# Kernel optimization log

Hardware: AMD Instinct MI355X
Metric: run time of the kernel (lower is better)

Reference implementation:

```python
import jax, jax.numpy as jnp
import numpy as np

N = 4096; IN = 78; OUT = 11
HN = 256; HB = 128; HM = 64; HV = 256; HU = 128
NOTES_PER_BEAT = 8; BEATS_PER_MEASURE = 4
NB = N // NOTES_PER_BEAT; NM = NB // BEATS_PER_MEASURE
UIN = 2*HN + 2*HB + 2*HM + 2*HV + OUT + 2 + 1 + 2   # output-LSTM input = 1424
BT_IN = 2*HB + 1 + 1 + 2 + 3 + (OUT - 1)            # tempo-LSTM input = 273
QPM_PRIMO_IDX = 5; TEMPO_IDX = 28


def _u(key, shape, k):
    return jax.random.uniform(key, shape, minval=-k, maxval=k, dtype=jnp.float32)


def _lstm_p(key, din, h, bidir):
    k = 1.0 / np.sqrt(h); n = 2 if bidir else 1
    k1, k2, k3 = jax.random.split(key, 3)
    Wi = _u(k1, (n, 4*h, din), k); Wh = _u(k2, (n, 4*h, h), k); b = _u(k3, (n, 4*h), k)
    if not bidir:
        Wi, Wh, b = Wi[0], Wh[0], b[0]
    return Wi, Wh, b


def _lin_p(key, din, dout):
    k = 1.0 / np.sqrt(din)
    k1, k2 = jax.random.split(key)
    return _u(k1, (dout, din), k), _u(k2, (dout,), k)


def setup_inputs():
    ks = jax.random.split(jax.random.key(0), 20)
    inp = {}
    inp['x'] = jax.random.normal(ks[0], (1, N, IN), dtype=jnp.float32)
    inp['y'] = jax.random.normal(ks[1], (1, 1, OUT), dtype=jnp.float32)
    inp['beat_ids'] = (jnp.arange(N) // NOTES_PER_BEAT).astype(jnp.int32)
    inp['measure_ids'] = (jnp.arange(N) // (NOTES_PER_BEAT * BEATS_PER_MEASURE)).astype(jnp.int32)
    inp['note_Wi'], inp['note_Wh'], inp['note_b'] = _lstm_p(ks[2], IN, HN, True)
    inp['voice_Wi'], inp['voice_Wh'], inp['voice_b'] = _lstm_p(ks[3], IN, HV, True)
    inp['beat_Wi'], inp['beat_Wh'], inp['beat_b'] = _lstm_p(ks[4], 2*HN, HB, True)
    inp['meas_Wi'], inp['meas_Wh'], inp['meas_b'] = _lstm_p(ks[5], 2*HB, HM, True)
    inp['Wba'], inp['bba'] = _lin_p(ks[6], 2*HN, 2*HN)
    inp['Wma'], inp['bma'] = _lin_p(ks[7], 2*HB, 2*HB)
    inp['Wta'], inp['bta'] = _lin_p(ks[8], OUT-1, OUT-1)
    inp['out_Wi'], inp['out_Wh'], inp['out_b'] = _lstm_p(ks[9], UIN, HU, False)
    inp['Wfc'], inp['bfc'] = _lin_p(ks[10], HU + UIN, OUT-1)
    inp['bt_Wi'], inp['bt_Wh'], inp['bt_b'] = _lstm_p(ks[11], BT_IN, HB, False)
    inp['Wt1'], inp['bt1'] = _lin_p(ks[12], HB, HB)
    inp['Wt2'], inp['bt2'] = _lin_p(ks[13], HB, 1)
    return inp


def _cell(h, c, xt, Wi, Wh, b):
    g = Wi @ xt + Wh @ h + b
    i, f, gg, o = jnp.split(g, 4)
    c2 = jax.nn.sigmoid(f) * c + jax.nn.sigmoid(i) * jnp.tanh(gg)
    return jax.nn.sigmoid(o) * jnp.tanh(c2), c2


def _lstm(xs, Wi, Wh, b, reverse=False):
    H = Wh.shape[-1]
    def step(carry, xt):
        h, c = _cell(carry[0], carry[1], xt, Wi, Wh, b)
        return (h, c), h
    init = (jnp.zeros(H, xs.dtype), jnp.zeros(H, xs.dtype))
    _, hs = jax.lax.scan(step, init, xs, reverse=reverse)
    return hs


def _bilstm(xs, Wi, Wh, b):
    return jnp.concatenate([_lstm(xs, Wi[0], Wh[0], b[0]),
                            _lstm(xs, Wi[1], Wh[1], b[1], reverse=True)], axis=-1)


def _seg_attn(h, seg, nseg, W, b):
    # sum_with_attention: softmax over group members, per feature dim (torch softmax dim=0)
    logits = h @ W.T + b
    m = jax.ops.segment_max(logits, seg, num_segments=nseg)
    e = jnp.exp(logits - m[seg])
    s = jax.ops.segment_sum(e, seg, num_segments=nseg)
    return jax.ops.segment_sum(h * (e / s[seg]), seg, num_segments=nseg)


def _forward(x, y, beat_ids, measure_ids, note_Wi, note_Wh, note_b, voice_Wi, voice_Wh, voice_b,
             beat_Wi, beat_Wh, beat_b, meas_Wi, meas_Wh, meas_b, Wba, bba, Wma, bma, Wta, bta,
             out_Wi, out_Wh, out_b, Wfc, bfc, bt_Wi, bt_Wh, bt_b, Wt1, bt1, Wt2, bt2):
    xs = x[0]                                   # [N, IN]
    note_h = _bilstm(xs, note_Wi, note_Wh, note_b)          # [N, 2*HN]
    voice_h = _bilstm(xs, voice_Wi, voice_Wh, voice_b)      # single voice -> whole seq
    beat_nodes = _seg_attn(note_h, beat_ids, NB, Wba, bba)  # [NB, 2*HN]
    beat_h = _bilstm(beat_nodes, beat_Wi, beat_Wh, beat_b)  # [NB, 2*HB]
    meas_of_beat = jax.ops.segment_min(measure_ids, beat_ids, num_segments=NB)
    meas_nodes = _seg_attn(beat_h, meas_of_beat, NM, Wma, bma)
    meas_h = _bilstm(meas_nodes, meas_Wi, meas_Wh, meas_b)  # [NM, 2*HM]

    qpm_primo = x[:, 0, QPM_PRIMO_IDX]          # (1,)
    tempo_primo = x[0, 0, -2:]                  # (2,)
    btv = xs[:, TEMPO_IDX:TEMPO_IDX+3]          # [N, 3]
    beat_pn = beat_h[beat_ids]                  # [N, 2*HB]
    meas_pn = meas_h[measure_ids]               # [N, 2*HM]
    is_b = jnp.concatenate([jnp.array([True]), beat_ids[1:] > beat_ids[:-1]])
    y_tail = y[0, 0, 1:]

    def step(carry, inp):
        buf, count, pt, th, tc, oh, oc, po, pv = carry
        nh_i, bh_i, mh_i, vh_i, btv_i, isb = inp
        # --- beat boundary: tempo attention + tempo LSTM step ---
        mask = jnp.arange(NOTES_PER_BEAT) < count
        logits = jnp.where(mask[:, None], buf @ Wta.T + bta, -1e9)
        att = jax.nn.softmax(logits, axis=0)
        result_node = jnp.where(count > 0, jnp.sum(buf * att, axis=0), y_tail)
        cat = jnp.concatenate([bh_i, pt, qpm_primo, tempo_primo, btv_i, result_node])
        nth, ntc = _cell(th, tc, cat, bt_Wi, bt_Wh, bt_b)
        tmp = Wt2 @ jax.nn.relu(Wt1 @ nth + bt1) + bt2     # (1,)
        th = jnp.where(isb, nth, th); tc = jnp.where(isb, ntc, tc)
        pt = jnp.where(isb, tmp, pt)
        buf = jnp.where(isb, jnp.zeros_like(buf), buf)
        count = jnp.where(isb, 0, count)
        comb = jnp.concatenate([nh_i, bh_i, mh_i, vh_i, po, pv, qpm_primo, tempo_primo])  # (UIN,)
        noh, noc = _cell(oh, oc, comb, out_Wi, out_Wh, out_b)
        out_fc = Wfc @ jnp.concatenate([noh, comb]) + bfc   # (OUT-1,)
        out = jnp.concatenate([pt, out_fc])                 # (OUT,)
        buf = buf.at[count].set(out_fc)
        return (buf, count + 1, pt, th, tc, noh, noc, out, out_fc[:2]), out

    carry0 = (jnp.zeros((NOTES_PER_BEAT, OUT-1)), jnp.array(0, jnp.int32), y[:, 0, 0],
              jnp.zeros(HB), jnp.zeros(HB), jnp.zeros(HU), jnp.zeros(HU), y[0, 0, :], jnp.zeros(2))
    _, outs = jax.lax.scan(step, carry0, (note_h, beat_pn, meas_pn, voice_h, btv, is_b))
    return outs[None], note_h[None]


def reference(x, y, beat_ids, measure_ids, note_Wi, note_Wh, note_b, voice_Wi, voice_Wh, voice_b,
              beat_Wi, beat_Wh, beat_b, meas_Wi, meas_Wh, meas_b, Wba, bba, Wma, bma, Wta, bta,
              out_Wi, out_Wh, out_b, Wfc, bfc, bt_Wi, bt_Wh, bt_b, Wt1, bt1, Wt2, bt2):
    return _forward(x, y, beat_ids, measure_ids, note_Wi, note_Wh, note_b, voice_Wi, voice_Wh, voice_b,
                    beat_Wi, beat_Wh, beat_b, meas_Wi, meas_Wh, meas_b, Wba, bba, Wma, bma, Wta, bta,
                    out_Wi, out_Wh, out_b, Wfc, bfc, bt_Wi, bt_Wh, bt_b, Wt1, bt1, Wt2, bt2)
```

## Files before the change

### kernel.cpp

```cpp
#include <hip/hip_runtime.h>
#include <hip/hip_bf16.h>

typedef unsigned int u32;
typedef _Float16 h16;
typedef __attribute__((ext_vector_type(2))) _Float16 h16x2;

union U4 { uint4 u; h16x2 p[4]; };

static __device__ __forceinline__ float sigm(float x){ return 1.0f / (1.0f + __expf(-x)); }
static __device__ __forceinline__ float ftanh(float x){ return 1.0f - 2.0f/(1.0f + __expf(2.0f*x)); }
static __device__ __forceinline__ h16x2 f2h2(float a, float b){
  h16x2 r; r[0] = (h16)a; r[1] = (h16)b; return r;
}
static __device__ __forceinline__ void pinv(h16x2 &x){
  u32 t = __builtin_bit_cast(u32, x);
  asm volatile("" : "+v"(t));
  x = __builtin_bit_cast(h16x2, t);
}

#if defined(__has_builtin)
#if __has_builtin(__builtin_amdgcn_fdot2)
#define FDOT2_NATIVE 1
#endif
#endif
static __device__ __forceinline__ float fdot2(h16x2 a, h16x2 b, float c){
#ifdef FDOT2_NATIVE
  return __builtin_amdgcn_fdot2(a, b, c, false);
#else
  return c + (float)a[0]*(float)b[0] + (float)a[1]*(float)b[1];
#endif
}

#define NT 4096
#define OUTS_OFF 45056

__global__ __launch_bounds__(256) void k0_prep(
    const float* __restrict__ noteWh, const float* __restrict__ voiceWh,
    const float* __restrict__ outWi,  const float* __restrict__ Wfc,
    h16* __restrict__ WhF, h16* __restrict__ outWiF, h16* __restrict__ WfcKF)
{
  const int NWH = 4*1024*256;
  const int NOW = 512*1416;
  const int NFC = 10*1416;
  for (int i = blockIdx.x*256 + threadIdx.x; i < NWH + NOW + NFC; i += gridDim.x*256) {
    if (i < NWH) {
      int dir = i >> 18;
      int rem = i & 262143;
      const float* src = (dir < 2) ? noteWh : voiceWh;
      WhF[i] = (h16)src[((dir & 1) << 18) + rem];
    } else if (i < NWH + NOW) {
      int j = i - NWH;
      int r = j / 1416, c = j - r*1416;
      float v = 0.f;
      if (c < 1408) v = outWi[(size_t)r*1424 + c];
      else if (c < 1411) v = outWi[(size_t)r*1424 + 1421 + (c-1408)];
      outWiF[j] = (h16)v;
    } else {
      int j = i - NWH - NOW;
      int r = j / 1416, c = j - r*1416;
      float v = 0.f;
      if (c < 1408) v = Wfc[(size_t)r*1552 + 128 + c];
      else if (c < 1411) v = Wfc[(size_t)r*1552 + 1549 + (c-1408)];
      WfcKF[j] = (h16)v;
    }
  }
}

__global__ __launch_bounds__(256) void k1_xgates(
    const float* __restrict__ x,
    const float* __restrict__ noteWi, const float* __restrict__ noteB,
    const float* __restrict__ voiceWi, const float* __restrict__ voiceB,
    h16* __restrict__ preNV)
{
  const int dir = blockIdx.y;
  const int t0  = blockIdx.x * 16;
  const int tid = threadIdx.x;
  __shared__ float xs[16][80];
  for (int i = tid; i < 16*78; i += 256) {
    int tt = i / 78, j = i - tt*78;
    xs[tt][j] = x[(size_t)(t0+tt)*78 + j];
  }
  __syncthreads();
  const float* Wi = (dir < 2) ? noteWi : voiceWi;
  const float* B  = (dir < 2) ? noteB  : voiceB;
  const int dw = dir & 1;
  for (int gc = 0; gc < 4; ++gc) {
    int g = gc*256 + tid;
    const float* row = Wi + ((size_t)dw*1024 + g)*78;
    float bias = B[dw*1024 + g];
    float acc[16];
#pragma unroll
    for (int tt=0; tt<16; ++tt) acc[tt] = bias;
#pragma unroll 6
    for (int j=0; j<78; ++j) {
      float w = row[j];
#pragma unroll
      for (int tt=0; tt<16; ++tt)
        acc[tt] += w*xs[tt][j];
    }
#pragma unroll
    for (int tt=0; tt<16; ++tt)
      preNV[((size_t)dir*NT + (t0+tt))*1024 + (tid*4 + gc)] = (h16)acc[tt];
  }
}

__global__ __launch_bounds__(512, 2) void k2_nvrec(
    const h16* __restrict__ WhF,
    const h16* __restrict__ preNV,
    float* __restrict__ note_h,
    float* __restrict__ voice_h,
    float* __restrict__ out_noteh)
{
  const int dir = blockIdx.x;
  const int L = threadIdx.x;
  const int lane = L & 63;
  const int wid  = L >> 6;
  const int hi   = lane >> 5;
  const int e    = wid*32 + (lane & 31);
  const int c0   = hi*128;
  const h16* Wb = WhF + (size_t)dir*1024*256;

  h16x2 w[4][48];
#pragma unroll
  for (int g=0; g<4; ++g) {
    const h16* row = Wb + (size_t)(g*256 + e)*256 + c0;
#pragma unroll
    for (int cb=0; cb<12; ++cb) {
      U4 a; a.u = *(const uint4*)(row + cb*8);
#pragma unroll
      for (int i=0;i<4;++i) w[g][cb*4+i] = a.p[i];
    }
  }
#pragma unroll
  for (int g=0; g<4; ++g)
#pragma unroll
    for (int c=0;c<48;++c) pinv(w[g][c]);

  __shared__ __align__(16) h16 Wl[4*4*2*256*8];
  __shared__ __align__(16) h16 hb[2][256];
#pragma unroll
  for (int cb=0; cb<4; ++cb)
#pragma unroll
    for (int g=0; g<4; ++g) {
      const h16* src = Wb + (size_t)(g*256 + e)*256 + c0 + 96 + cb*8;
      *(uint4*)&Wl[(size_t)((((cb*4+g)*2 + hi)*256 + e))*8] = *(const uint4*)src;
    }
  if (hi == 0) hb[0][e] = (h16)0.f;
  float cc = 0.f;
  __syncthreads();

  const bool fwd = ((dir & 1) == 0);
  const bool isNote = (dir < 2);
  float* hout = isNote ? note_h : voice_h;
  const int half = (dir & 1) * 256;
  const h16* pre = preNV + (size_t)dir*NT*1024;
  int cur = 0;
  const int step = fwd ? 1 : -1;
  int t = fwd ? 0 : NT-1;

  union PU { uint2 u; h16 h[4]; };
  PU pv_n; pv_n.u = *(const uint2*)(pre + (size_t)t*1024 + e*4);

  for (int it = 0; it < NT; ++it, t += step) {
    PU pv = pv_n;
    if (it+1 < NT) pv_n.u = *(const uint2*)(pre + (size_t)(t+step)*1024 + e*4);

    float ac[4][2] = {{0.f,0.f},{0.f,0.f},{0.f,0.f},{0.f,0.f}};
#pragma unroll
    for (int cb=0; cb<12; ++cb) {
      U4 hh; hh.u = *(const uint4*)&hb[cur][c0 + cb*8];
#pragma unroll
      for (int i=0;i<4;++i) {
        ac[0][i&1] = fdot2(w[0][cb*4+i], hh.p[i], ac[0][i&1]);
        ac[1][i&1] = fdot2(w[1][cb*4+i], hh.p[i], ac[1][i&1]);
        ac[2][i&1] = fdot2(w[2][cb*4+i], hh.p[i], ac[2][i&1]);
        ac[3][i&1] = fdot2(w[3][cb*4+i], hh.p[i], ac[3][i&1]);
      }
    }
#pragma unroll
    for (int cb=0; cb<4; ++cb) {
      U4 hh; hh.u = *(const uint4*)&hb[cur][c0 + 96 + cb*8];
#pragma unroll
      for (int g=0; g<4; ++g) {
        U4 wv; wv.u = *(const uint4*)&Wl[(size_t)((((cb*4+g)*2 + hi)*256 + e))*8];
#pragma unroll
        for (int i=0;i<4;++i) ac[g][i&1] = fdot2(wv.p[i], hh.p[i], ac[g][i&1]);
      }
    }
    float g4[4];
#pragma unroll
    for (int g=0; g<4; ++g) {
      float s = ac[g][0] + ac[g][1];
      s += __shfl_xor(s, 32, 64);
      g4[g] = s;
    }
    float gi = (float)pv.h[0] + g4[0];
    float gf = (float)pv.h[1] + g4[1];
    float gg = (float)pv.h[2] + g4[2];
    float go = (float)pv.h[3] + g4[3];
    cc = sigm(gf)*cc + sigm(gi)*ftanh(gg);
    float h = sigm(go)*ftanh(cc);
    if (hi == 0) {
      hb[cur^1][e] = (h16)h;
      hout[(size_t)t*512 + half + e] = h;
      if (isNote) out_noteh[(size_t)t*512 + half + e] = h;
    }
    cur ^= 1;
    __syncthreads();
  }
}

__global__ __launch_bounds__(256) void k3_battn(
    const float* __restrict__ note_h,
    const float* __restrict__ Wba, const float* __restrict__ bba,
    float* __restrict__ beat_nodes)
{
  const int b = blockIdx.x;
  const int tid = threadIdx.x;
  __shared__ float nh[8][512];
  for (int i = tid; i < 8*512; i += 256)
    nh[i>>9][i&511] = note_h[(size_t)b*8*512 + i];
  __syncthreads();
  for (int dc = 0; dc < 2; ++dc) {
    int d = dc*256 + tid;
    const float* wr = Wba + (size_t)d*512;
    float bb = bba[d];
    float l[8];
#pragma unroll
    for (int n=0;n<8;++n) l[n]=bb;
#pragma unroll 4
    for (int j=0; j<512; ++j) {
      float w = wr[j];
#pragma unroll
      for (int n=0;n<8;++n) l[n] += w*nh[n][j];
    }
    float m = l[0];
#pragma unroll
    for (int n=1;n<8;++n) m = fmaxf(m, l[n]);
    float s = 0.f, o = 0.f;
#pragma unroll
    for (int n=0;n<8;++n) { float e = __expf(l[n]-m); s += e; o += e*nh[n][d]; }
    beat_nodes[(size_t)b*512 + d] = o / s;
  }
}

__global__ __launch_bounds__(256) void k4_bgates(
    const float* __restrict__ beat_nodes,
    const float* __restrict__ beatWi, const float* __restrict__ beatB,
    float* __restrict__ preB)
{
  const int dir = blockIdx.y, b0 = blockIdx.x*8, tid = threadIdx.x;
  __shared__ float nd[8][512];
  for (int i = tid; i < 8*512; i += 256)
    nd[i>>9][i&511] = beat_nodes[(size_t)b0*512 + i];
  __syncthreads();
  for (int gc = 0; gc < 2; ++gc) {
    int g = gc*256 + tid;
    const float* wr = beatWi + ((size_t)dir*512 + g)*512;
    float bias = beatB[dir*512 + g];
    float acc[8];
#pragma unroll
    for (int n=0;n<8;++n) acc[n]=bias;
#pragma unroll 4
    for (int j=0; j<512; ++j) {
      float w = wr[j];
#pragma unroll
      for (int n=0;n<8;++n) acc[n] += w*nd[n][j];
    }
#pragma unroll
    for (int n=0;n<8;++n)
      preB[((size_t)dir*512 + (b0+n))*512 + g] = acc[n];
  }
}

__global__ __launch_bounds__(512) void k5_brec(
    const float* __restrict__ beatWh,
    const float* __restrict__ preB,
    float* __restrict__ beat_h)
{
  const int dir = blockIdx.x, L = threadIdx.x;
  h16x2 w[64];
  {
    const float2* p = (const float2*)(beatWh + ((size_t)dir*512 + L)*128);
#pragma unroll
    for (int c=0;c<64;++c){
      float2 v = p[c];
      w[c] = f2h2(v.x, v.y);
    }
  }
#pragma unroll
  for (int c=0;c<64;++c) pinv(w[c]);
  __shared__ __align__(16) h16 hb[128];
  __shared__ float gl[512];
  if (L < 128) hb[L] = (h16)0.f;
  float cc = 0.f;
  __syncthreads();
  const bool fwd = (dir == 0);
  for (int it = 0; it < 512; ++it) {
    const int t = fwd ? it : 511 - it;
    float pr = preB[((size_t)dir*512 + t)*512 + L];
    float ac[4] = {0.f,0.f,0.f,0.f};
#pragma unroll
    for (int c=0;c<16;++c){
      U4 hh; hh.u = *(const uint4*)&hb[c*8];
#pragma unroll
      for (int i=0;i<4;++i) ac[i] = fdot2(w[c*4+i], hh.p[i], ac[i]);
    }
    gl[L] = pr + ((ac[0]+ac[1]) + (ac[2]+ac[3]));
    __syncthreads();
    if (L < 128) {
      float gi = gl[L], gf = gl[L+128], gg = gl[L+256], go = gl[L+384];
      cc = sigm(gf)*cc + sigm(gi)*ftanh(gg);
      float h = sigm(go)*ftanh(cc);
      hb[L] = (h16)h;
      beat_h[(size_t)t*256 + dir*128 + L] = h;
    }
    __syncthreads();
  }
}

__global__ __launch_bounds__(256) void k6_mattn(
    const float* __restrict__ beat_h,
    const float* __restrict__ Wma, const float* __restrict__ bma,
    float* __restrict__ meas_nodes)
{
  const int m = blockIdx.x, tid = threadIdx.x;
  __shared__ float bh[4][256];
  for (int i = tid; i < 4*256; i += 256)
    bh[i>>8][i&255] = beat_h[(size_t)m*4*256 + i];
  __syncthreads();
  int d = tid;
  const float* wr = Wma + (size_t)d*256;
  float bb = bma[d];
  float l[4];
#pragma unroll
  for (int n=0;n<4;++n) l[n]=bb;
#pragma unroll 4
  for (int j=0; j<256; ++j) {
    float w = wr[j];
#pragma unroll
    for (int n=0;n<4;++n) l[n] += w*bh[n][j];
  }
  float mm = fmaxf(fmaxf(l[0],l[1]), fmaxf(l[2],l[3]));
  float s = 0.f, o = 0.f;
#pragma unroll
  for (int n=0;n<4;++n) { float e = __expf(l[n]-mm); s += e; o += e*bh[n][d]; }
  meas_nodes[(size_t)m*256 + d] = o / s;
}

__global__ __launch_bounds__(256) void k7_mgates(
    const float* __restrict__ meas_nodes,
    const float* __restrict__ measWi, const float* __restrict__ measB,
    float* __restrict__ preM)
{
  const int dir = blockIdx.y, m0 = blockIdx.x*8, tid = threadIdx.x;
  __shared__ float nd[8][256];
  for (int i = tid; i < 8*256; i += 256)
    nd[i>>8][i&255] = meas_nodes[(size_t)m0*256 + i];
  __syncthreads();
  int g = tid;
  const float* wr = measWi + ((size_t)dir*256 + g)*256;
  float bias = measB[dir*256 + g];
  float acc[8];
#pragma unroll
  for (int n=0;n<8;++n) acc[n]=bias;
#pragma unroll 4
  for (int j=0; j<256; ++j) {
    float w = wr[j];
#pragma unroll
    for (int n=0;n<8;++n) acc[n] += w*nd[n][j];
  }
#pragma unroll
  for (int n=0;n<8;++n)
    preM[((size_t)dir*128 + (m0+n))*256 + g] = acc[n];
}

__global__ __launch_bounds__(256, 2) void k8_mrec(
    const float* __restrict__ measWh,
    const float* __restrict__ preM,
    float* __restrict__ meas_h)
{
  const int dir = blockIdx.x, L = threadIdx.x;
  h16x2 w[32];
  {
    const float2* p = (const float2*)(measWh + ((size_t)dir*256 + L)*64);
#pragma unroll
    for (int c=0;c<32;++c){
      float2 v = p[c];
      w[c] = f2h2(v.x, v.y);
    }
  }
#pragma unroll
  for (int c=0;c<32;++c) pinv(w[c]);
  __shared__ __align__(16) h16 hb[64];
  __shared__ float gl[256];
  if (L < 64) hb[L] = (h16)0.f;
  float cc = 0.f;
  __syncthreads();
  const bool fwd = (dir == 0);
  for (int it = 0; it < 128; ++it) {
    const int t = fwd ? it : 127 - it;
    float pr = preM[((size_t)dir*128 + t)*256 + L];
    float ac[4] = {0.f,0.f,0.f,0.f};
#pragma unroll
    for (int c=0;c<8;++c){
      U4 hh; hh.u = *(const uint4*)&hb[c*8];
#pragma unroll
      for (int i=0;i<4;++i) ac[i] = fdot2(w[c*4+i], hh.p[i], ac[i]);
    }
    gl[L] = pr + ((ac[0]+ac[1]) + (ac[2]+ac[3]));
    __syncthreads();
    if (L < 64) {
      float gi = gl[L], gf = gl[L+64], gg = gl[L+128], go = gl[L+192];
      cc = sigm(gf)*cc + sigm(gi)*ftanh(gg);
      float h = sigm(go)*ftanh(cc);
      hb[L] = (h16)h;
      meas_h[(size_t)t*128 + dir*64 + L] = h;
    }
    __syncthreads();
  }
}

__global__ __launch_bounds__(256) void k9_scanpre(
    const float* __restrict__ note_h, const float* __restrict__ voice_h,
    const float* __restrict__ beat_h, const float* __restrict__ meas_h,
    const float* __restrict__ xf,
    const h16* __restrict__ outWiF, const h16* __restrict__ WfcKF,
    const float* __restrict__ outB, const float* __restrict__ bfc,
    float* __restrict__ pre_out, float* __restrict__ pre_fc)
{
  const int t0 = blockIdx.x*8, tid = threadIdx.x;
  __shared__ __align__(16) h16 kn[8][1416];
  const float qpm = xf[5], tp0 = xf[76], tp1 = xf[77];
  for (int i = tid; i < 8*1416; i += 256) {
    int tt = i/1416, c = i - tt*1416;
    int t = t0 + tt;
    float v;
    if (c < 512) v = note_h[(size_t)t*512 + c];
    else if (c < 768) v = beat_h[(size_t)(t>>3)*256 + (c-512)];
    else if (c < 896) v = meas_h[(size_t)(t>>5)*128 + (c-768)];
    else if (c < 1408) v = voice_h[(size_t)t*512 + (c-896)];
    else if (c == 1408) v = qpm;
    else if (c == 1409) v = tp0;
    else if (c == 1410) v = tp1;
    else v = 0.f;
    kn[tt][c] = (h16)v;
  }
  __syncthreads();
  for (int rr = 0; rr < 3; ++rr) {
    int r = (rr < 2) ? (tid + rr*256) : (512 + tid);
    if (rr == 2 && tid >= 10) break;
    const h16* wrow = (r < 512) ? (outWiF + (size_t)r*1416) : (WfcKF + (size_t)(r-512)*1416);
    float bias = (r < 512) ? outB[r] : bfc[r-512];
    float acc[8];
#pragma unroll
    for (int tt=0;tt<8;++tt) acc[tt] = bias;
    for (int cu = 0; cu < 177; ++cu) {
      U4 wv; wv.u = *(const uint4*)(wrow + cu*8);
#pragma unroll
      for (int tt=0; tt<8; ++tt) {
        U4 kv; kv.u = *(const uint4*)&kn[tt][cu*8];
#pragma unroll
        for (int i=0;i<4;++i) acc[tt] = fdot2(wv.p[i], kv.p[i], acc[tt]);
      }
    }
#pragma unroll
    for (int tt=0; tt<8; ++tt) {
      if (r < 512) pre_out[(size_t)(t0+tt)*512 + r] = acc[tt];
      else pre_fc[(size_t)(t0+tt)*16 + (r-512)] = acc[tt];
    }
  }
}

__global__ __launch_bounds__(256) void k9b_btpre(
    const float* __restrict__ beat_h, const float* __restrict__ xf,
    const float* __restrict__ btWi, const float* __restrict__ btB,
    float* __restrict__ pre_bt)
{
  const int b0 = blockIdx.x*8, tid = threadIdx.x;
  __shared__ float bh[8][256];
  __shared__ float btv[8][3];
  for (int i = tid; i < 8*256; i += 256)
    bh[i>>8][i&255] = beat_h[(size_t)b0*256 + i];
  if (tid < 24) {
    int n = tid/3, j = tid - n*3;
    btv[n][j] = xf[(size_t)(b0+n)*8*78 + 28 + j];
  }
  __syncthreads();
  const float qpm = xf[5], tp0 = xf[76], tp1 = xf[77];
  for (int gc = 0; gc < 2; ++gc) {
    int g = gc*256 + tid;
    const float* row = btWi + (size_t)g*273;
    float bias = btB[g];
    float acc[8];
#pragma unroll
    for (int n=0;n<8;++n) acc[n]=bias;
#pragma unroll 4
    for (int j = 0; j < 256; ++j) {
      float w = row[j];
#pragma unroll
      for (int n=0;n<8;++n) acc[n] += w*bh[n][j];
    }
    float w257 = row[257], w258 = row[258], w259 = row[259];
    float w260 = row[260], w261 = row[261], w262 = row[262];
#pragma unroll
    for (int n=0;n<8;++n) {
      acc[n] += w257*qpm + w258*tp0 + w259*tp1
              + w260*btv[n][0] + w261*btv[n][1] + w262*btv[n][2];
      pre_bt[(size_t)(b0+n)*512 + g] = acc[n];
    }
  }
}

__global__ __launch_bounds__(512) void k10_scan(
    const float* __restrict__ pre_out, const float* __restrict__ pre_fc,
    const float* __restrict__ pre_bt,
    const float* __restrict__ outWh, const float* __restrict__ btWh,
    const float* __restrict__ outWi, const float* __restrict__ btWi,
    const float* __restrict__ Wfc,
    const float* __restrict__ Wta, const float* __restrict__ bta,
    const float* __restrict__ Wt1, const float* __restrict__ bt1,
    const float* __restrict__ Wt2, const float* __restrict__ bt2,
    const float* __restrict__ yf,
    float* __restrict__ out)
{
  const int L = threadIdx.x;
  h16x2 owh[64], btw[64];
  {
    const float2* p = (const float2*)(outWh + (size_t)L*128);
    const float2* q = (const float2*)(btWh + (size_t)L*128);
#pragma unroll
    for (int c=0;c<64;++c){
      float2 a = p[c]; owh[c] = f2h2(a.x, a.y);
      float2 b = q[c]; btw[c] = f2h2(b.x, b.y);
    }
  }
#pragma unroll
  for (int c=0;c<64;++c){ pinv(owh[c]); pinv(btw[c]); }
  float oseq[13];
#pragma unroll
  for (int j=0;j<13;++j) oseq[j] = outWi[(size_t)L*1424 + 1408 + j];
  float btpt = btWi[(size_t)L*273 + 256];
  float btrn[10];
#pragma unroll
  for (int d=0;d<10;++d) btrn[d] = btWi[(size_t)L*273 + 263 + d];

  __shared__ __align__(16) h16 oh16[128];
  __shared__ __align__(16) h16 th16[128];
  __shared__ __align__(16) h16 Wt1f[128*136];
  __shared__ __align__(16) h16 WfcD[10*128];
  __shared__ float gl[512], gb[512];
  __shared__ float pofc[16];
  __shared__ float ptvS;
  __shared__ float buf[8][10];
  __shared__ float rn[10], att[8][10], r1v[128], ytail[10];
  __shared__ float WfcSeq[10][13];
  __shared__ float WtaS[100], btaS[10], Wt2S[128], bt1S[128], bt2S;

  for (int i=L; i<128*128; i+=512) Wt1f[(i>>7)*136 + (i&127)] = (h16)Wt1[i];
  for (int i=L; i<10*128; i+=512)  WfcD[i] = (h16)Wfc[(size_t)(i>>7)*1552 + (i&127)];
  if (L < 100) WtaS[L] = Wta[L];
  if (L < 10)  btaS[L] = bta[L];
  if (L < 128) { Wt2S[L] = Wt2[L]; bt1S[L] = bt1[L]; }
  if (L == 0)  bt2S = bt2[0];
  if (L < 128) { oh16[L] = (h16)0.f; th16[L] = (h16)0.f; }
  if (L < 11) pofc[L] = yf[L];
  if (L >= 11 && L < 16) pofc[L] = 0.f;
  if (L == 0) ptvS = yf[0];
  if (L < 10) ytail[L] = yf[1+L];
  if (L < 80) buf[L/10][L%10] = 0.f;
  if (L < 130) WfcSeq[L/13][L%13] = Wfc[(size_t)(L/13)*1552 + 1536 + (L%13)];
  float oc = 0.f, tc = 0.f;
  const int dD = L >> 2, qD = L & 3;
  float prv  = pre_out[L];
  float prbt = pre_bt[L];
  float prfc = (L < 40 && qD == 0) ? pre_fc[dD] : 0.f;
  __syncthreads();

  for (int t = 0; t < NT; ++t) {
    const bool isb = (t & 7) == 0;
    if (isb) {
      if (t == 0) {
        if (L < 10) rn[L] = ytail[L];
      } else {
        if (L < 80) {
          int n = L/10, d = L - n*10;
          float s = btaS[d];
#pragma unroll
          for (int j=0;j<10;++j) s += buf[n][j]*WtaS[d*10 + j];
          att[n][d] = s;
        }
        __syncthreads();
        if (L < 10) {
          float m = att[0][L];
#pragma unroll
          for (int n=1;n<8;++n) m = fmaxf(m, att[n][L]);
          float s = 0.f, acc = 0.f;
#pragma unroll
          for (int n=0;n<8;++n) { float e = __expf(att[n][L]-m); s += e; acc += e*buf[n][L]; }
          rn[L] = acc/s;
        }
      }
      __syncthreads();
    }
    {
      float pr = prv;
      if (t+1 < NT) prv = pre_out[(size_t)(t+1)*512 + L];
      float ac[4] = {0.f,0.f,0.f,0.f};
#pragma unroll
      for (int c=0;c<16;++c){
        U4 hh; hh.u = *(const uint4*)&oh16[c*8];
#pragma unroll
        for (int i=0;i<4;++i) ac[i] = fdot2(owh[c*4+i], hh.p[i], ac[i]);
      }
      float a = pr + ((ac[0]+ac[1]) + (ac[2]+ac[3]));
#pragma unroll
      for (int j=0;j<13;++j) a += oseq[j]*pofc[j];
      gl[L] = a;
    }
    if (isb) {
      float pr = prbt + btpt*ptvS;
      if (t+8 < NT) prbt = pre_bt[(size_t)((t>>3)+1)*512 + L];
      float ac[4] = {0.f,0.f,0.f,0.f};
#pragma unroll
      for (int c=0;c<16;++c){
        U4 hh; hh.u = *(const uint4*)&th16[c*8];
#pragma unroll
        for (int i=0;i<4;++i) ac[i] = fdot2(btw[c*4+i], hh.p[i], ac[i]);
      }
      float b = pr + ((ac[0]+ac[1]) + (ac[2]+ac[3]));
#pragma unroll
      for (int d=0;d<10;++d) b += btrn[d]*rn[d];
      gb[L] = b;
    }
    __syncthreads();
    if (L < 128) {
      float gi = gl[L], gf = gl[L+128], gg = gl[L+256], go = gl[L+384];
      oc = sigm(gf)*oc + sigm(gi)*ftanh(gg);
      float nh = sigm(go)*ftanh(oc);
      oh16[L] = (h16)nh;
    } else if (L < 256 && isb) {
      int j = L - 128;
      float gi = gb[j], gf = gb[j+128], gg = gb[j+256], go = gb[j+384];
      tc = sigm(gf)*tc + sigm(gi)*ftanh(gg);
      float nth = sigm(go)*ftanh(tc);
      th16[j] = (h16)nth;
    }
    __syncthreads();
    if (isb) {
      if (L < 128) {
        float ac[4] = {0.f,0.f,0.f,0.f};
        const h16* wrow = &Wt1f[L*136];
#pragma unroll
        for (int k=0;k<16;++k){
          U4 wv; wv.u = *(const uint4*)(wrow + k*8);
          U4 hh; hh.u = *(const uint4*)&th16[k*8];
#pragma unroll
          for (int i=0;i<4;++i) ac[i] = fdot2(wv.p[i], hh.p[i], ac[i]);
        }
        float s = bt1S[L] + ((ac[0]+ac[1]) + (ac[2]+ac[3]));
        r1v[L] = fmaxf(s, 0.f);
      }
      __syncthreads();
    }
    if (L < 64) {
      float ptv_l;
      if (isb) {
        float p = Wt2S[L]*r1v[L] + Wt2S[L+64]*r1v[L+64];
#pragma unroll
        for (int sft=32; sft>0; sft>>=1) p += __shfl_xor(p, sft, 64);
        ptv_l = p + bt2S;
        if (L == 0) ptvS = ptv_l;
      } else {
        ptv_l = ptvS;
      }
      float s = 0.f;
      if (L < 40) {
        const h16* wr = &WfcD[dD*128 + qD*32];
#pragma unroll
        for (int j=0;j<32;++j) s += (float)wr[j] * (float)oh16[qD*32 + j];
      }
      s += __shfl_xor(s, 1, 64);
      s += __shfl_xor(s, 2, 64);
      float e = 0.f;
      if (L < 40 && qD == 0) {
        e = prfc;
#pragma unroll
        for (int j=0;j<13;++j) e += WfcSeq[dD][j]*pofc[j];
        if (t+1 < NT) prfc = pre_fc[(size_t)(t+1)*16 + dD];
      }
      float ofc = s + e;
      int srcE = (L >= 1 && L < 11) ? 4*(L-1) : ((L >= 11 && L < 13) ? 4*(L-11) : 0);
      float valE = __shfl(ofc, srcE, 64);
      float bval = __shfl(ofc, 4*(L & 15), 64);
      if (L == 0)      { out[(size_t)t*11] = ptv_l; pofc[0] = ptv_l; }
      else if (L < 11) { out[(size_t)t*11 + L] = valE; pofc[L] = valE; }
      else if (L < 13) { pofc[L] = valE; }
      if (L < 10) buf[t & 7][L] = bval;
    }
    __syncthreads();
  }
}

extern "C" void kernel_launch(void* const* d_in, const int* in_sizes, int n_in,
                              void* d_out, int out_size, void* d_ws, size_t ws_size,
                              hipStream_t stream)
{
  const float* x      = (const float*)d_in[0];
  const float* y      = (const float*)d_in[1];
  const float* noteWi = (const float*)d_in[4];
  const float* noteWh = (const float*)d_in[5];
  const float* noteB  = (const float*)d_in[6];
  const float* voiceWi= (const float*)d_in[7];
  const float* voiceWh= (const float*)d_in[8];
  const float* voiceB = (const float*)d_in[9];
  const float* beatWi = (const float*)d_in[10];
  const float* beatWh = (const float*)d_in[11];
  const float* beatB  = (const float*)d_in[12];
  const float* measWi = (const float*)d_in[13];
  const float* measWh = (const float*)d_in[14];
  const float* measB  = (const float*)d_in[15];
  const float* Wba    = (const float*)d_in[16];
  const float* bba    = (const float*)d_in[17];
  const float* Wma    = (const float*)d_in[18];
  const float* bma    = (const float*)d_in[19];
  const float* Wta    = (const float*)d_in[20];
  const float* bta    = (const float*)d_in[21];
  const float* outWi  = (const float*)d_in[22];
  const float* outWh  = (const float*)d_in[23];
  const float* outB   = (const float*)d_in[24];
  const float* Wfc    = (const float*)d_in[25];
  const float* bfc    = (const float*)d_in[26];
  const float* btWi   = (const float*)d_in[27];
  const float* btWh   = (const float*)d_in[28];
  const float* btB    = (const float*)d_in[29];
  const float* Wt1    = (const float*)d_in[30];
  const float* bt1    = (const float*)d_in[31];
  const float* Wt2    = (const float*)d_in[32];
  const float* bt2    = (const float*)d_in[33];

  float* fws = (float*)d_ws;
  float* note_h     = fws + 0;
  float* voice_h    = fws + 2097152;
  float* beat_nodes = fws + 4194304;
  float* preB       = fws + 4456448;
  float* beat_h     = fws + 4980736;
  float* meas_nodes = fws + 5111808;
  float* preM       = fws + 5144576;
  float* meas_h     = fws + 5210112;
  float* pre_out    = fws + 5226496;
  float* pre_fc     = fws + 7323648;
  float* pre_bt     = fws + 7389184;
  h16* hws   = (h16*)(fws + 7651328);
  h16* preNV  = hws;
  h16* WhF    = hws + 16777216;
  h16* outWiF = hws + 17825792;
  h16* WfcKF  = hws + 18550784;

  float* out_outs  = (float*)d_out;
  float* out_noteh = out_outs + OUTS_OFF;

  hipLaunchKernelGGL(k0_prep, dim3(1024), dim3(256), 0, stream,
                     noteWh, voiceWh, outWi, Wfc, WhF, outWiF, WfcKF);
  hipLaunchKernelGGL(k1_xgates, dim3(256,4), dim3(256), 0, stream,
                     x, noteWi, noteB, voiceWi, voiceB, preNV);
  hipLaunchKernelGGL(k2_nvrec, dim3(4), dim3(512), 0, stream,
                     WhF, preNV, note_h, voice_h, out_noteh);
  hipLaunchKernelGGL(k3_battn, dim3(512), dim3(256), 0, stream,
                     note_h, Wba, bba, beat_nodes);
  hipLaunchKernelGGL(k4_bgates, dim3(64,2), dim3(256), 0, stream,
                     beat_nodes, beatWi, beatB, preB);
  hipLaunchKernelGGL(k5_brec, dim3(2), dim3(512), 0, stream,
                     beatWh, preB, beat_h);
  hipLaunchKernelGGL(k6_mattn, dim3(128), dim3(256), 0, stream,
                     beat_h, Wma, bma, meas_nodes);
  hipLaunchKernelGGL(k7_mgates, dim3(16,2), dim3(256), 0, stream,
                     meas_nodes, measWi, measB, preM);
  hipLaunchKernelGGL(k8_mrec, dim3(2), dim3(256), 0, stream,
                     measWh, preM, meas_h);
  hipLaunchKernelGGL(k9b_btpre, dim3(64), dim3(256), 0, stream,
                     beat_h, x, btWi, btB, pre_bt);
  hipLaunchKernelGGL(k9_scanpre, dim3(512), dim3(256), 0, stream,
                     note_h, voice_h, beat_h, meas_h, x, outWiF, WfcKF, outB, bfc, pre_out, pre_fc);
  hipLaunchKernelGGL(k10_scan, dim3(1), dim3(512), 0, stream,
                     pre_out, pre_fc, pre_bt, outWh, btWh, outWi, btWi, Wfc,
                     Wta, bta, Wt1, bt1, Wt2, bt2, y, out_outs);
}
```

Baseline: 14.80 ms.

## Use one thread per hidden unit in note/voice recurrence, drop cross-half shuffle

```diff
diff --git a/kernel.cpp b/kernel.cpp
--- a/kernel.cpp
+++ b/kernel.cpp
@@ -104,7 +104,7 @@
   }
 }
 
-__global__ __launch_bounds__(512, 2) void k2_nvrec(
+__global__ __launch_bounds__(256, 1) void k2_nvrec(
     const h16* __restrict__ WhF,
     const h16* __restrict__ preNV,
     float* __restrict__ note_h,
@@ -112,20 +112,15 @@
     float* __restrict__ out_noteh)
 {
   const int dir = blockIdx.x;
-  const int L = threadIdx.x;
-  const int lane = L & 63;
-  const int wid  = L >> 6;
-  const int hi   = lane >> 5;
-  const int e    = wid*32 + (lane & 31);
-  const int c0   = hi*128;
+  const int e = threadIdx.x;
   const h16* Wb = WhF + (size_t)dir*1024*256;
 
-  h16x2 w[4][48];
+  h16x2 w[4][96];
 #pragma unroll
   for (int g=0; g<4; ++g) {
-    const h16* row = Wb + (size_t)(g*256 + e)*256 + c0;
-#pragma unroll
-    for (int cb=0; cb<12; ++cb) {
+    const h16* row = Wb + (size_t)(g*256 + e)*256;
+#pragma unroll
+    for (int cb=0; cb<24; ++cb) {
       U4 a; a.u = *(const uint4*)(row + cb*8);
 #pragma unroll
       for (int i=0;i<4;++i) w[g][cb*4+i] = a.p[i];
@@ -134,18 +129,18 @@
 #pragma unroll
   for (int g=0; g<4; ++g)
 #pragma unroll
-    for (int c=0;c<48;++c) pinv(w[g][c]);
-
-  __shared__ __align__(16) h16 Wl[4*4*2*256*8];
+    for (int c=0;c<96;++c) pinv(w[g][c]);
+
+  __shared__ __align__(16) h16 Wl[8*4*256*8];
   __shared__ __align__(16) h16 hb[2][256];
 #pragma unroll
-  for (int cb=0; cb<4; ++cb)
+  for (int blk=0; blk<8; ++blk)
 #pragma unroll
     for (int g=0; g<4; ++g) {
-      const h16* src = Wb + (size_t)(g*256 + e)*256 + c0 + 96 + cb*8;
-      *(uint4*)&Wl[(size_t)((((cb*4+g)*2 + hi)*256 + e))*8] = *(const uint4*)src;
-    }
-  if (hi == 0) hb[0][e] = (h16)0.f;
+      const h16* src = Wb + (size_t)(g*256 + e)*256 + 192 + blk*8;
+      *(uint4*)&Wl[(size_t)(((blk*4+g)*256 + e))*8] = *(const uint4*)src;
+    }
+  hb[0][e] = (h16)0.f;
   float cc = 0.f;
   __syncthreads();
 
@@ -167,8 +162,8 @@
 
     float ac[4][2] = {{0.f,0.f},{0.f,0.f},{0.f,0.f},{0.f,0.f}};
 #pragma unroll
-    for (int cb=0; cb<12; ++cb) {
-      U4 hh; hh.u = *(const uint4*)&hb[cur][c0 + cb*8];
+    for (int cb=0; cb<24; ++cb) {
+      U4 hh; hh.u = *(const uint4*)&hb[cur][cb*8];
 #pragma unroll
       for (int i=0;i<4;++i) {
         ac[0][i&1] = fdot2(w[0][cb*4+i], hh.p[i], ac[0][i&1]);
@@ -178,33 +173,24 @@
       }
     }
 #pragma unroll
-    for (int cb=0; cb<4; ++cb) {
-      U4 hh; hh.u = *(const uint4*)&hb[cur][c0 + 96 + cb*8];
+    for (int blk=0; blk<8; ++blk) {
+      U4 hh; hh.u = *(const uint4*)&hb[cur][192 + blk*8];
 #pragma unroll
       for (int g=0; g<4; ++g) {
-        U4 wv; wv.u = *(const uint4*)&Wl[(size_t)((((cb*4+g)*2 + hi)*256 + e))*8];
+        U4 wv; wv.u = *(const uint4*)&Wl[(size_t)(((blk*4+g)*256 + e))*8];
 #pragma unroll
         for (int i=0;i<4;++i) ac[g][i&1] = fdot2(wv.p[i], hh.p[i], ac[g][i&1]);
       }
     }
-    float g4[4];
-#pragma unroll
-    for (int g=0; g<4; ++g) {
-      float s = ac[g][0] + ac[g][1];
-      s += __shfl_xor(s, 32, 64);
-      g4[g] = s;
-    }
-    float gi = (float)pv.h[0] + g4[0];
-    float gf = (float)pv.h[1] + g4[1];
-    float gg = (float)pv.h[2] + g4[2];
-    float go = (float)pv.h[3] + g4[3];
+    float gi = (float)pv.h[0] + ac[0][0] + ac[0][1];
+    float gf = (float)pv.h[1] + ac[1][0] + ac[1][1];
+    float gg = (float)pv.h[2] + ac[2][0] + ac[2][1];
+    float go = (float)pv.h[3] + ac[3][0] + ac[3][1];
     cc = sigm(gf)*cc + sigm(gi)*ftanh(gg);
     float h = sigm(go)*ftanh(cc);
-    if (hi == 0) {
-      hb[cur^1][e] = (h16)h;
-      hout[(size_t)t*512 + half + e] = h;
-      if (isNote) out_noteh[(size_t)t*512 + half + e] = h;
-    }
+    hb[cur^1][e] = (h16)h;
+    hout[(size_t)t*512 + half + e] = h;
+    if (isNote) out_noteh[(size_t)t*512 + half + e] = h;
     cur ^= 1;
     __syncthreads();
   }
@@ -764,7 +750,7 @@
                      noteWh, voiceWh, outWi, Wfc, WhF, outWiF, WfcKF);
   hipLaunchKernelGGL(k1_xgates, dim3(256,4), dim3(256), 0, stream,
                      x, noteWi, noteB, voiceWi, voiceB, preNV);
-  hipLaunchKernelGGL(k2_nvrec, dim3(4), dim3(512), 0, stream,
+  hipLaunchKernelGGL(k2_nvrec, dim3(4), dim3(256), 0, stream,
                      WhF, preNV, note_h, voice_h, out_noteh);
   hipLaunchKernelGGL(k3_battn, dim3(512), dim3(256), 0, stream,
                      note_h, Wba, bba, beat_nodes);
```

After: 19.82 ms. 1.34x slower.

## Precompute recurrent matvecs at end of previous scan step, tune waves-per-EU

Applied to the files above, without the earlier changes.

```diff
diff --git a/kernel.cpp b/kernel.cpp
--- a/kernel.cpp
+++ b/kernel.cpp
@@ -104,7 +104,8 @@
   }
 }
 
-__global__ __launch_bounds__(512, 2) void k2_nvrec(
+__global__ __launch_bounds__(512) __attribute__((amdgpu_waves_per_eu(2, 2)))
+void k2_nvrec(
     const h16* __restrict__ WhF,
     const h16* __restrict__ preNV,
     float* __restrict__ note_h,
@@ -512,7 +513,8 @@
   }
 }
 
-__global__ __launch_bounds__(512) void k10_scan(
+__global__ __launch_bounds__(512) __attribute__((amdgpu_waves_per_eu(2, 2)))
+void k10_scan(
     const float* __restrict__ pre_out, const float* __restrict__ pre_fc,
     const float* __restrict__ pre_bt,
     const float* __restrict__ outWh, const float* __restrict__ btWh,
@@ -550,7 +552,7 @@
   __shared__ __align__(16) h16 Wt1f[128*136];
   __shared__ __align__(16) h16 WfcD[10*128];
   __shared__ float gl[512], gb[512];
-  __shared__ float pofc[16];
+  __shared__ __align__(16) float pofc[16];
   __shared__ float ptvS;
   __shared__ float buf[8][10];
   __shared__ float rn[10], att[8][10], r1v[128], ytail[10];
@@ -575,6 +577,10 @@
   float prv  = pre_out[L];
   float prbt = pre_bt[L];
   float prfc = (L < 40 && qD == 0) ? pre_fc[dD] : 0.f;
+  const float* pp_out = pre_out + 512 + L;
+  const float* pp_bt  = pre_bt  + 512 + L;
+  const float* pp_fc  = pre_fc  + 16 + dD;
+  float acA = 0.f, acB = 0.f;
   __syncthreads();
 
   for (int t = 0; t < NT; ++t) {
@@ -604,34 +610,24 @@
       __syncthreads();
     }
     {
-      float pr = prv;
-      if (t+1 < NT) prv = pre_out[(size_t)(t+1)*512 + L];
-      float ac[4] = {0.f,0.f,0.f,0.f};
-#pragma unroll
-      for (int c=0;c<16;++c){
-        U4 hh; hh.u = *(const uint4*)&oh16[c*8];
-#pragma unroll
-        for (int i=0;i<4;++i) ac[i] = fdot2(owh[c*4+i], hh.p[i], ac[i]);
-      }
-      float a = pr + ((ac[0]+ac[1]) + (ac[2]+ac[3]));
-#pragma unroll
-      for (int j=0;j<13;++j) a += oseq[j]*pofc[j];
+      float4 p0 = *(const float4*)&pofc[0];
+      float4 p1 = *(const float4*)&pofc[4];
+      float4 p2 = *(const float4*)&pofc[8];
+      float  pc = pofc[12];
+      float a = prv + acA;
+      a += oseq[0]*p0.x + oseq[1]*p0.y + oseq[2]*p0.z + oseq[3]*p0.w;
+      a += oseq[4]*p1.x + oseq[5]*p1.y + oseq[6]*p1.z + oseq[7]*p1.w;
+      a += oseq[8]*p2.x + oseq[9]*p2.y + oseq[10]*p2.z + oseq[11]*p2.w;
+      a += oseq[12]*pc;
       gl[L] = a;
+      prv = *pp_out; pp_out += 512;
     }
     if (isb) {
-      float pr = prbt + btpt*ptvS;
-      if (t+8 < NT) prbt = pre_bt[(size_t)((t>>3)+1)*512 + L];
-      float ac[4] = {0.f,0.f,0.f,0.f};
-#pragma unroll
-      for (int c=0;c<16;++c){
-        U4 hh; hh.u = *(const uint4*)&th16[c*8];
-#pragma unroll
-        for (int i=0;i<4;++i) ac[i] = fdot2(btw[c*4+i], hh.p[i], ac[i]);
-      }
-      float b = pr + ((ac[0]+ac[1]) + (ac[2]+ac[3]));
+      float b = prbt + btpt*ptvS + acB;
 #pragma unroll
       for (int d=0;d<10;++d) b += btrn[d]*rn[d];
       gb[L] = b;
+      prbt = *pp_bt; pp_bt += 512;
     }
     __syncthreads();
     if (L < 128) {
@@ -687,7 +683,7 @@
         e = prfc;
 #pragma unroll
         for (int j=0;j<13;++j) e += WfcSeq[dD][j]*pofc[j];
-        if (t+1 < NT) prfc = pre_fc[(size_t)(t+1)*16 + dD];
+        prfc = *pp_fc; pp_fc += 16;
       }
       float ofc = s + e;
       int srcE = (L >= 1 && L < 11) ? 4*(L-1) : ((L >= 11 && L < 13) ? 4*(L-11) : 0);
@@ -697,6 +693,30 @@
       else if (L < 11) { out[(size_t)t*11 + L] = valE; pofc[L] = valE; }
       else if (L < 13) { pofc[L] = valE; }
       if (L < 10) buf[t & 7][L] = bval;
+    }
+    {
+      float a0=0.f,a1=0.f,a2=0.f,a3=0.f;
+#pragma unroll
+      for (int c=0;c<16;++c){
+        U4 hh; hh.u = *(const uint4*)&oh16[c*8];
+        a0 = fdot2(owh[c*4+0], hh.p[0], a0);
+        a1 = fdot2(owh[c*4+1], hh.p[1], a1);
+        a2 = fdot2(owh[c*4+2], hh.p[2], a2);
+        a3 = fdot2(owh[c*4+3], hh.p[3], a3);
+      }
+      acA = (a0+a1) + (a2+a3);
+    }
+    if (((t+1) & 7) == 0) {
+      float b0=0.f,b1=0.f,b2=0.f,b3=0.f;
+#pragma unroll
+      for (int c=0;c<16;++c){
+        U4 hh; hh.u = *(const uint4*)&th16[c*8];
+        b0 = fdot2(btw[c*4+0], hh.p[0], b0);
+        b1 = fdot2(btw[c*4+1], hh.p[1], b1);
+        b2 = fdot2(btw[c*4+2], hh.p[2], b2);
+        b3 = fdot2(btw[c*4+3], hh.p[3], b3);
+      }
+      acB = (b0+b1) + (b2+b3);
     }
     __syncthreads();
   }
```

Measured after the change: 14.49 ms. 1.02x faster.

## Restructure serial scan so each thread owns all four gates of one hidden unit

Applied to the files above, without the earlier changes.

```diff
diff --git a/kernel.cpp b/kernel.cpp
--- a/kernel.cpp
+++ b/kernel.cpp
@@ -104,7 +104,8 @@
   }
 }
 
-__global__ __launch_bounds__(512, 2) void k2_nvrec(
+__global__ __launch_bounds__(512) __attribute__((amdgpu_waves_per_eu(2, 2)))
+void k2_nvrec(
     const h16* __restrict__ WhF,
     const h16* __restrict__ preNV,
     float* __restrict__ note_h,
@@ -466,7 +467,7 @@
     }
 #pragma unroll
     for (int tt=0; tt<8; ++tt) {
-      if (r < 512) pre_out[(size_t)(t0+tt)*512 + r] = acc[tt];
+      if (r < 512) pre_out[((size_t)(t0+tt)*128 + (r & 127))*4 + (r >> 7)] = acc[tt];
       else pre_fc[(size_t)(t0+tt)*16 + (r-512)] = acc[tt];
     }
   }
@@ -507,12 +508,13 @@
     for (int n=0;n<8;++n) {
       acc[n] += w257*qpm + w258*tp0 + w259*tp1
               + w260*btv[n][0] + w261*btv[n][1] + w262*btv[n][2];
-      pre_bt[(size_t)(b0+n)*512 + g] = acc[n];
-    }
-  }
-}
-
-__global__ __launch_bounds__(512) void k10_scan(
+      pre_bt[((size_t)(b0+n)*128 + (g & 127))*4 + (g >> 7)] = acc[n];
+    }
+  }
+}
+
+__global__ __launch_bounds__(512) __attribute__((amdgpu_waves_per_eu(2, 2)))
+void k10_scan(
     const float* __restrict__ pre_out, const float* __restrict__ pre_fc,
     const float* __restrict__ pre_bt,
     const float* __restrict__ outWh, const float* __restrict__ btWh,
@@ -525,32 +527,42 @@
     float* __restrict__ out)
 {
   const int L = threadIdx.x;
-  h16x2 owh[64], btw[64];
-  {
-    const float2* p = (const float2*)(outWh + (size_t)L*128);
-    const float2* q = (const float2*)(btWh + (size_t)L*128);
-#pragma unroll
-    for (int c=0;c<64;++c){
-      float2 a = p[c]; owh[c] = f2h2(a.x, a.y);
-      float2 b = q[c]; btw[c] = f2h2(b.x, b.y);
-    }
-  }
-#pragma unroll
-  for (int c=0;c<64;++c){ pinv(owh[c]); pinv(btw[c]); }
+  const int lane = L & 63;
+  const int wid  = L >> 6;
+  const int jl   = lane & 15;
+  const int q    = lane >> 4;
+  const int j    = wid*16 + jl;
+  const int row  = q*128 + j;
+
+  h16x2 owh[4][16], btw[4][16];
+#pragma unroll
+  for (int g=0; g<4; ++g) {
+    const float2* p  = (const float2*)(outWh + (size_t)(g*128 + j)*128 + q*32);
+    const float2* pb = (const float2*)(btWh  + (size_t)(g*128 + j)*128 + q*32);
+#pragma unroll
+    for (int c=0;c<16;++c){
+      float2 a = p[c];  owh[g][c] = f2h2(a.x, a.y);
+      float2 b = pb[c]; btw[g][c] = f2h2(b.x, b.y);
+    }
+  }
+#pragma unroll
+  for (int g=0; g<4; ++g)
+#pragma unroll
+    for (int c=0;c<16;++c) pinv(owh[g][c]);
+
   float oseq[13];
 #pragma unroll
-  for (int j=0;j<13;++j) oseq[j] = outWi[(size_t)L*1424 + 1408 + j];
-  float btpt = btWi[(size_t)L*273 + 256];
+  for (int jj=0;jj<13;++jj) oseq[jj] = outWi[(size_t)row*1424 + 1408 + jj];
+  float btpt = btWi[(size_t)row*273 + 256];
   float btrn[10];
 #pragma unroll
-  for (int d=0;d<10;++d) btrn[d] = btWi[(size_t)L*273 + 263 + d];
+  for (int d=0;d<10;++d) btrn[d] = btWi[(size_t)row*273 + 263 + d];
 
   __shared__ __align__(16) h16 oh16[128];
   __shared__ __align__(16) h16 th16[128];
   __shared__ __align__(16) h16 Wt1f[128*136];
   __shared__ __align__(16) h16 WfcD[10*128];
-  __shared__ float gl[512], gb[512];
-  __shared__ float pofc[16];
+  __shared__ __align__(16) float pofc[16];
   __shared__ float ptvS;
   __shared__ float buf[8][10];
   __shared__ float rn[10], att[8][10], r1v[128], ytail[10];
@@ -571,10 +583,15 @@
   if (L < 80) buf[L/10][L%10] = 0.f;
   if (L < 130) WfcSeq[L/13][L%13] = Wfc[(size_t)(L/13)*1552 + 1536 + (L%13)];
   float oc = 0.f, tc = 0.f;
+  float ac4[4]  = {0.f,0.f,0.f,0.f};
+  float acB4[4] = {0.f,0.f,0.f,0.f};
   const int dD = L >> 2, qD = L & 3;
-  float prv  = pre_out[L];
-  float prbt = pre_bt[L];
+  const float* ppo = pre_out + (size_t)j*4 + q;
+  const float* ppb = pre_bt  + (size_t)j*4 + q;
+  float prv  = *ppo; ppo += 512;
+  float prbt = *ppb; ppb += 512;
   float prfc = (L < 40 && qD == 0) ? pre_fc[dD] : 0.f;
+  const float* pp_fc = pre_fc + 16 + dD;
   __syncthreads();
 
   for (int t = 0; t < NT; ++t) {
@@ -587,7 +604,7 @@
           int n = L/10, d = L - n*10;
           float s = btaS[d];
 #pragma unroll
-          for (int j=0;j<10;++j) s += buf[n][j]*WtaS[d*10 + j];
+          for (int jj=0;jj<10;++jj) s += buf[n][jj]*WtaS[d*10 + jj];
           att[n][d] = s;
         }
         __syncthreads();
@@ -604,49 +621,76 @@
       __syncthreads();
     }
     {
-      float pr = prv;
-      if (t+1 < NT) prv = pre_out[(size_t)(t+1)*512 + L];
-      float ac[4] = {0.f,0.f,0.f,0.f};
-#pragma unroll
-      for (int c=0;c<16;++c){
-        U4 hh; hh.u = *(const uint4*)&oh16[c*8];
-#pragma unroll
-        for (int i=0;i<4;++i) ac[i] = fdot2(owh[c*4+i], hh.p[i], ac[i]);
-      }
-      float a = pr + ((ac[0]+ac[1]) + (ac[2]+ac[3]));
-#pragma unroll
-      for (int j=0;j<13;++j) a += oseq[j]*pofc[j];
-      gl[L] = a;
+      float4 pf0 = *(const float4*)&pofc[0];
+      float4 pf1 = *(const float4*)&pofc[4];
+      float4 pf2 = *(const float4*)&pofc[8];
+      float  pcc = pofc[12];
+      float ex = prv;
+      ex += oseq[0]*pf0.x + oseq[1]*pf0.y + oseq[2]*pf0.z + oseq[3]*pf0.w;
+      ex += oseq[4]*pf1.x + oseq[5]*pf1.y + oseq[6]*pf1.z + oseq[7]*pf1.w;
+      ex += oseq[8]*pf2.x + oseq[9]*pf2.y + oseq[10]*pf2.z + oseq[11]*pf2.w;
+      ex += oseq[12]*pcc;
+      prv = *ppo; ppo += 512;
+      float p0 = ac4[0] + ((q==0) ? ex : 0.f);
+      float p1 = ac4[1] + ((q==1) ? ex : 0.f);
+      float p2 = ac4[2] + ((q==2) ? ex : 0.f);
+      float p3 = ac4[3] + ((q==3) ? ex : 0.f);
+      p0 += __shfl_xor(p0, 16, 64); p0 += __shfl_xor(p0, 32, 64);
+      p1 += __shfl_xor(p1, 16, 64); p1 += __shfl_xor(p1, 32, 64);
+      p2 += __shfl_xor(p2, 16, 64); p2 += __shfl_xor(p2, 32, 64);
+      p3 += __shfl_xor(p3, 16, 64); p3 += __shfl_xor(p3, 32, 64);
+      oc = sigm(p1)*oc + sigm(p0)*ftanh(p2);
+      float nh = sigm(p3)*ftanh(oc);
+      if (q == 0) oh16[j] = (h16)nh;
     }
     if (isb) {
-      float pr = prbt + btpt*ptvS;
-      if (t+8 < NT) prbt = pre_bt[(size_t)((t>>3)+1)*512 + L];
-      float ac[4] = {0.f,0.f,0.f,0.f};
-#pragma unroll
-      for (int c=0;c<16;++c){
-        U4 hh; hh.u = *(const uint4*)&th16[c*8];
-#pragma unroll
-        for (int i=0;i<4;++i) ac[i] = fdot2(btw[c*4+i], hh.p[i], ac[i]);
-      }
-      float b = pr + ((ac[0]+ac[1]) + (ac[2]+ac[3]));
-#pragma unroll
-      for (int d=0;d<10;++d) b += btrn[d]*rn[d];
-      gb[L] = b;
+      float ex = prbt + btpt*ptvS;
+#pragma unroll
+      for (int d=0;d<10;++d) ex += btrn[d]*rn[d];
+      prbt = *ppb; ppb += 512;
+      float p0 = acB4[0] + ((q==0) ? ex : 0.f);
+      float p1 = acB4[1] + ((q==1) ? ex : 0.f);
+      float p2 = acB4[2] + ((q==2) ? ex : 0.f);
+      float p3 = acB4[3] + ((q==3) ? ex : 0.f);
+      p0 += __shfl_xor(p0, 16, 64); p0 += __shfl_xor(p0, 32, 64);
+      p1 += __shfl_xor(p1, 16, 64); p1 += __shfl_xor(p1, 32, 64);
+      p2 += __shfl_xor(p2, 16, 64); p2 += __shfl_xor(p2, 32, 64);
+      p3 += __shfl_xor(p3, 16, 64); p3 += __shfl_xor(p3, 32, 64);
+      tc = sigm(p1)*tc + sigm(p0)*ftanh(p2);
+      float nth = sigm(p3)*ftanh(tc);
+      if (q == 0) th16[j] = (h16)nth;
     }
     __syncthreads();
-    if (L < 128) {
-      float gi = gl[L], gf = gl[L+128], gg = gl[L+256], go = gl[L+384];
-      oc = sigm(gf)*oc + sigm(gi)*ftanh(gg);
-      float nh = sigm(go)*ftanh(oc);
-      oh16[L] = (h16)nh;
-    } else if (L < 256 && isb) {
-      int j = L - 128;
-      float gi = gb[j], gf = gb[j+128], gg = gb[j+256], go = gb[j+384];
-      tc = sigm(gf)*tc + sigm(gi)*ftanh(gg);
-      float nth = sigm(go)*ftanh(tc);
-      th16[j] = (h16)nth;
-    }
-    __syncthreads();
+    {
+      float a0=0.f,a1=0.f,a2=0.f,a3=0.f;
+#pragma unroll
+      for (int cb=0; cb<4; ++cb) {
+        U4 hh; hh.u = *(const uint4*)&oh16[q*32 + cb*8];
+#pragma unroll
+        for (int i=0;i<4;++i) {
+          a0 = fdot2(owh[0][cb*4+i], hh.p[i], a0);
+          a1 = fdot2(owh[1][cb*4+i], hh.p[i], a1);
+          a2 = fdot2(owh[2][cb*4+i], hh.p[i], a2);
+          a3 = fdot2(owh[3][cb*4+i], hh.p[i], a3);
+        }
+      }
+      ac4[0]=a0; ac4[1]=a1; ac4[2]=a2; ac4[3]=a3;
+    }
+    if (((t+1) & 7) == 0) {
+      float b0=0.f,b1=0.f,b2=0.f,b3=0.f;
+#pragma unroll
+      for (int cb=0; cb<4; ++cb) {
+        U4 hh; hh.u = *(const uint4*)&th16[q*32 + cb*8];
+#pragma unroll
+        for (int i=0;i<4;++i) {
+          b0 = fdot2(btw[0][cb*4+i], hh.p[i], b0);
+          b1 = fdot2(btw[1][cb*4+i], hh.p[i], b1);
+          b2 = fdot2(btw[2][cb*4+i], hh.p[i], b2);
+          b3 = fdot2(btw[3][cb*4+i], hh.p[i], b3);
+        }
+      }
+      acB4[0]=b0; acB4[1]=b1; acB4[2]=b2; acB4[3]=b3;
+    }
     if (isb) {
       if (L < 128) {
         float ac[4] = {0.f,0.f,0.f,0.f};
@@ -678,7 +722,7 @@
       if (L < 40) {
         const h16* wr = &WfcD[dD*128 + qD*32];
 #pragma unroll
-        for (int j=0;j<32;++j) s += (float)wr[j] * (float)oh16[qD*32 + j];
+        for (int jj=0;jj<32;++jj) s += (float)wr[jj] * (float)oh16[qD*32 + jj];
       }
       s += __shfl_xor(s, 1, 64);
       s += __shfl_xor(s, 2, 64);
@@ -686,8 +730,8 @@
       if (L < 40 && qD == 0) {
         e = prfc;
 #pragma unroll
-        for (int j=0;j<13;++j) e += WfcSeq[dD][j]*pofc[j];
-        if (t+1 < NT) prfc = pre_fc[(size_t)(t+1)*16 + dD];
+        for (int jj=0;jj<13;++jj) e += WfcSeq[dD][jj]*pofc[jj];
+        prfc = *pp_fc; pp_fc += 16;
       }
       float ofc = s + e;
       int srcE = (L >= 1 && L < 11) ? 4*(L-1) : ((L >= 11 && L < 13) ? 4*(L-11) : 0);
```

Result: faster. 14.03 ms (-5.3%).
